# Optimization experiments

Measured on AMD Instinct MI355X. Metric: run time of the kernel, lower is better.

## Reference

```python
import jax, jax.numpy as jnp
import numpy as np

B, C, H, W = 16, 64, 32, 32
N_TOTAL = C * H * W          # 65536 flattened spatial units
N = 8192                     # samples_per_batch
EPS = 1e-12


def setup_inputs() -> dict:
    key = jax.random.key(0)
    k1, k2, k3 = jax.random.split(key, 3)
    layer_feature = jax.random.normal(k1, (B, C, H, W), dtype=jnp.float32)
    coordinates = jax.random.normal(k2, (N_TOTAL, 2), dtype=jnp.float32)
    # stand-in for torch.randperm(CHW)[:N]: unique in-range indices
    sampled_indices = jax.random.permutation(k3, N_TOTAL)[:N].astype(jnp.int64)
    return {"layer_feature": layer_feature, "coordinates": coordinates,
            "sampled_indices": sampled_indices}


def _masked_pearson(a, b, mask):
    # Pearson correlation between the masked (strict lower-triangle) entries
    cnt = jnp.sum(mask.astype(a.dtype))
    am = jnp.sum(jnp.where(mask, a, 0.0)) / cnt
    bm = jnp.sum(jnp.where(mask, b, 0.0)) / cnt
    ac = jnp.where(mask, a - am, 0.0)
    bc = jnp.where(mask, b - bm, 0.0)
    return jnp.sum(ac * bc) / (jnp.sqrt(jnp.sum(ac * ac)) * jnp.sqrt(jnp.sum(bc * bc)))


def reference(layer_feature, coordinates, sampled_indices):
    b = layer_feature.shape[0]
    feature = layer_feature.reshape(b, -1)[:, sampled_indices]   # [B, N]
    coords = coordinates[sampled_indices]                         # [N, 2]
    n = feature.shape[1]

    # distance similarity: 1 / (pdist + 1), full NxN (lower tri used)
    sq_norm = jnp.sum(coords * coords, axis=1)                    # [N]
    sq = sq_norm[:, None] + sq_norm[None, :] - 2.0 * (coords @ coords.T)
    sq = jnp.maximum(sq, 0.0)
    dist = jnp.sqrt(jnp.where(sq > EPS, sq, EPS))                 # safe sqrt
    distance_similarity = 1.0 / (dist + 1.0)                      # [N, N]

    # response similarity: corrcoef of feature.T -> NxN correlation over B
    X = feature.T                                                 # [N, B]
    Xc = X - jnp.mean(X, axis=1, keepdims=True)
    Xn = Xc / jnp.sqrt(jnp.sum(Xc * Xc, axis=1, keepdims=True))
    response_similarity = Xn @ Xn.T                               # [N, N]

    mask = jnp.tril(jnp.ones((n, n), dtype=bool), k=-1)           # strict lower tri
    similarity_alignment = _masked_pearson(response_similarity,
                                           distance_similarity, mask)
    return (1.0 - similarity_alignment) / 2.0
```

## Files before the change

kernel.cpp:

```cpp
#include <hip/hip_runtime.h>
#include <hip/hip_bf16.h>
#include <math.h>

#define NSAMP 8192
#define BATCH 16
#define CHW   65536
#define EPS_F 1e-12f

#define BT    128
#define NBT   (NSAMP / BT)
#define NINT  (NBT * (NBT - 1) / 2)
#define NBLK  (NINT + NBT)

typedef __attribute__((ext_vector_type(8))) short short8v;
typedef __attribute__((ext_vector_type(4))) float f32x4;
typedef __attribute__((ext_vector_type(2))) float f32x2;

#define OFF_XA 86016
#define OFF_C2 (OFF_XA + NSAMP * 32 * 2)

__global__ void __launch_bounds__(256)
prep_kernel(const float* __restrict__ feat, const float* __restrict__ coords,
            const int* __restrict__ sidx,
            __hip_bfloat16* __restrict__ XA, float* __restrict__ C2) {
    int t = blockIdx.x * 256 + threadIdx.x;
    int n = t >> 4, b = t & 15;
    int id = sidx[n];
    float v = feat[b * CHW + id];

    float m = v;
    m += __shfl_xor(m, 1, 16); m += __shfl_xor(m, 2, 16);
    m += __shfl_xor(m, 4, 16); m += __shfl_xor(m, 8, 16);
    float c = v - m * (1.0f / 16.0f);
    float q = c * c;
    q += __shfl_xor(q, 1, 16); q += __shfl_xor(q, 2, 16);
    q += __shfl_xor(q, 4, 16); q += __shfl_xor(q, 8, 16);
    float x = c * (1.0f / sqrtf(q));

    __hip_bfloat16 hi = __float2bfloat16(x);
    float hif = __bfloat162float(hi);
    __hip_bfloat16 lo = __float2bfloat16(x - hif);

    XA[n * 32 + b]      = hi;
    XA[n * 32 + 16 + b] = lo;
    if (b == 0) {
        float2 cc = reinterpret_cast<const float2*>(coords)[id];
        reinterpret_cast<float2*>(C2)[n] = cc;
    }
}

template<bool DIAG>
__device__ __forceinline__ void
compute_tiles(const short* __restrict__ XAs, const float* __restrict__ C2,
              int iW, int jW, int wi, int wj, int col, int kg, int rb,
              f32x2& vSa, f32x2& vSb, f32x2& vSab, f32x2& vSaa, f32x2& vSbb) {
    short8v afr[4], bhl[4], blh[4];
    f32x2 cix[4][2], ciy[4][2];
    float2 cj[4];
#pragma unroll
    for (int ti = 0; ti < 4; ++ti) {
        int rowA = iW + ti * 16 + col;
        afr[ti] = *reinterpret_cast<const short8v*>(XAs + rowA * 32 + kg * 8);
        const float4* cp =
            reinterpret_cast<const float4*>(C2 + (iW + ti * 16 + rb) * 2);
        float4 ca = cp[0], cb = cp[1];
        cix[ti][0] = (f32x2){ca.x, ca.z};  ciy[ti][0] = (f32x2){ca.y, ca.w};
        cix[ti][1] = (f32x2){cb.x, cb.z};  ciy[ti][1] = (f32x2){cb.y, cb.w};
    }
#pragma unroll
    for (int tj = 0; tj < 4; ++tj) {
        int rowB = jW + tj * 16 + col;
        bhl[tj] = *reinterpret_cast<const short8v*>(XAs + rowB * 32 + kg * 8);
        blh[tj] = *reinterpret_cast<const short8v*>(XAs + rowB * 32 + ((kg ^ 2) * 8));
        cj[tj]  = reinterpret_cast<const float2*>(C2)[rowB];
    }

#pragma unroll
    for (int tj = 0; tj < 4; ++tj) {
        const int gj = jW + tj * 16 + col;
        const f32x2 cjx = {cj[tj].x, cj[tj].x};
        const f32x2 cjy = {cj[tj].y, cj[tj].y};
        f32x4 acc[4];
#pragma unroll
        for (int ti = 0; ti < 4; ++ti) {
            if (DIAG && wi == wj && ti < tj) continue;
            f32x4 z = {0.f, 0.f, 0.f, 0.f};
            z = __builtin_amdgcn_mfma_f32_16x16x32_bf16(afr[ti], bhl[tj], z, 0, 0, 0);
            z = __builtin_amdgcn_mfma_f32_16x16x32_bf16(afr[ti], blh[tj], z, 0, 0, 0);
            acc[ti] = z;
        }
#pragma unroll
        for (int ti = 0; ti < 4; ++ti) {
            if (DIAG && wi == wj && ti < tj) continue;
            const int giB = iW + ti * 16 + rb;
#pragma unroll
            for (int p = 0; p < 2; ++p) {
                f32x2 av = {acc[ti][2 * p], acc[ti][2 * p + 1]};
                f32x2 dx = cix[ti][p] - cjx;
                f32x2 dy = ciy[ti][p] - cjy;
                f32x2 s2 = dx * dx + dy * dy;
                s2.x = fmaxf(s2.x, EPS_F);
                s2.y = fmaxf(s2.y, EPS_F);
                f32x2 d1;
                d1.x = __builtin_amdgcn_sqrtf(s2.x);
                d1.y = __builtin_amdgcn_sqrtf(s2.y);
                d1 = d1 + (f32x2){1.0f, 1.0f};
                f32x2 bb;
                bb.x = __builtin_amdgcn_rcpf(d1.x);
                bb.y = __builtin_amdgcn_rcpf(d1.y);
                f32x2 am = av;
                if (DIAG) {
                    f32x2 mk = {(giB + 2 * p + 0) > gj ? 1.0f : 0.0f,
                                (giB + 2 * p + 1) > gj ? 1.0f : 0.0f};
                    bb *= mk;
                    am *= mk;
                }
                vSa += am;
                vSb += bb;
                vSab += av * bb;
                vSaa += am * am;
                vSbb += bb * bb;
            }
        }
    }
}

template<bool DIAG>
__global__ void __launch_bounds__(256)
pair_kernel(const __hip_bfloat16* __restrict__ XA,
            const float* __restrict__ C2,
            double* __restrict__ partials) {
    int bi, bj, slot;
    if (DIAG) {
        bi = bj = blockIdx.x; slot = NINT + blockIdx.x;
    } else {
        int t = blockIdx.x;
        int e = (int)((1.0f + sqrtf(1.0f + 8.0f * (float)t)) * 0.5f);
        while (e * (e - 1) / 2 > t) --e;
        while ((e + 1) * e / 2 <= t) ++e;
        bi = e; bj = t - e * (e - 1) / 2; slot = t;
    }
    const int tid = threadIdx.x;
    const int wid = tid >> 6, l = tid & 63;
    const int wi = wid >> 1, wj = wid & 1;
    const int col = l & 15, kg = l >> 4, rb = kg * 4;

    const int iW = bi * BT + wi * 64;
    const int jW = bj * BT + wj * 64;

    f32x2 vSa = {0.f, 0.f}, vSb = {0.f, 0.f}, vSab = {0.f, 0.f};
    f32x2 vSaa = {0.f, 0.f}, vSbb = {0.f, 0.f};

    if (!(DIAG && wj > wi)) {
        const short* XAs = reinterpret_cast<const short*>(XA);
        compute_tiles<DIAG>(XAs, C2, iW, jW, wi, wj, col, kg, rb,
                            vSa, vSb, vSab, vSaa, vSbb);
    }

    double dSa  = (double)vSa.x  + (double)vSa.y;
    double dSb  = (double)vSb.x  + (double)vSb.y;
    double dSab = (double)vSab.x + (double)vSab.y;
    double dSaa = (double)vSaa.x + (double)vSaa.y;
    double dSbb = (double)vSbb.x + (double)vSbb.y;
#pragma unroll
    for (int o = 32; o > 0; o >>= 1) {
        dSa  += __shfl_down(dSa,  o, 64);
        dSb  += __shfl_down(dSb,  o, 64);
        dSab += __shfl_down(dSab, o, 64);
        dSaa += __shfl_down(dSaa, o, 64);
        dSbb += __shfl_down(dSbb, o, 64);
    }
    __shared__ double red[4][5];
    if (l == 0) {
        red[wid][0] = dSa;  red[wid][1] = dSb;  red[wid][2] = dSab;
        red[wid][3] = dSaa; red[wid][4] = dSbb;
    }
    __syncthreads();
    if (tid == 0) {
#pragma unroll
        for (int q = 0; q < 5; ++q)
            partials[slot * 5 + q] =
                red[0][q] + red[1][q] + red[2][q] + red[3][q];
    }
}

__global__ void __launch_bounds__(256)
finish_kernel(const double* __restrict__ partials, float* __restrict__ out) {
    double s0 = 0, s1 = 0, s2 = 0, s3 = 0, s4 = 0;
    for (int b = threadIdx.x; b < NBLK; b += 256) {
        s0 += partials[b * 5 + 0]; s1 += partials[b * 5 + 1];
        s2 += partials[b * 5 + 2]; s3 += partials[b * 5 + 3];
        s4 += partials[b * 5 + 4];
    }
    const int lane = threadIdx.x & 63, wid = threadIdx.x >> 6;
#pragma unroll
    for (int o = 32; o > 0; o >>= 1) {
        s0 += __shfl_down(s0, o, 64); s1 += __shfl_down(s1, o, 64);
        s2 += __shfl_down(s2, o, 64); s3 += __shfl_down(s3, o, 64);
        s4 += __shfl_down(s4, o, 64);
    }
    __shared__ double red[4][5];
    if (lane == 0) {
        red[wid][0] = s0; red[wid][1] = s1; red[wid][2] = s2;
        red[wid][3] = s3; red[wid][4] = s4;
    }
    __syncthreads();
    if (threadIdx.x == 0) {
        double Sa  = red[0][0] + red[1][0] + red[2][0] + red[3][0];
        double Sb  = red[0][1] + red[1][1] + red[2][1] + red[3][1];
        double Sab = red[0][2] + red[1][2] + red[2][2] + red[3][2];
        double Saa = red[0][3] + red[1][3] + red[2][3] + red[3][3];
        double Sbb = red[0][4] + red[1][4] + red[2][4] + red[3][4];
        const double cnt = (double)NSAMP * (double)(NSAMP - 1) * 0.5;
        double am = Sa / cnt, bm = Sb / cnt;
        double cov = Sab - cnt * am * bm;
        double va  = Saa - cnt * am * am;
        double vb  = Sbb - cnt * bm * bm;
        double corr = cov / (sqrt(va) * sqrt(vb));
        out[0] = (float)((1.0 - corr) * 0.5);
    }
}

extern "C" void kernel_launch(void* const* d_in, const int* in_sizes, int n_in,
                              void* d_out, int out_size, void* d_ws, size_t ws_size,
                              hipStream_t stream) {
    const float* feat   = (const float*)d_in[0];
    const float* coords = (const float*)d_in[1];
    const int*   sidx   = (const int*)d_in[2];
    float* out = (float*)d_out;

    double* partials = (double*)d_ws;
    __hip_bfloat16* XA = (__hip_bfloat16*)((char*)d_ws + OFF_XA);
    float* C2 = (float*)((char*)d_ws + OFF_C2);

    prep_kernel<<<NSAMP * BATCH / 256, 256, 0, stream>>>(feat, coords, sidx,
                                                         XA, C2);
    pair_kernel<false><<<NINT, 256, 0, stream>>>(XA, C2, partials);
    pair_kernel<true><<<NBT, 256, 0, stream>>>(XA, C2, partials);
    finish_kernel<<<1, 256, 0, stream>>>(partials, out);
}
```

Before: 87.48 us.

## Stage block tiles in padded LDS and fuse MFMA with epilogue

Each block now copies its 128-row A and B slices of the split-bf16 features, plus their coordinates, into padded shared memory (row stride 40 shorts) before computing. The per-wave fragment loads then read from LDS instead of global/L2, so the four waves share one copy of each tile. The MFMA and the similarity epilogue are fused per tile so no accumulator array is kept, the EPS clamp before sqrt is dropped, and launch bounds request 4 blocks per CU. The price is an extra LDS round trip and a __syncthreads per block. Without the clamp, coincident coordinates give sqrt(0) rather than sqrt(EPS), which should change the result only negligibly.

```diff
diff --git a/kernel.cpp b/kernel.cpp
--- a/kernel.cpp
+++ b/kernel.cpp
@@ -5,12 +5,13 @@
 #define NSAMP 8192
 #define BATCH 16
 #define CHW   65536
-#define EPS_F 1e-12f
 
 #define BT    128
 #define NBT   (NSAMP / BT)
 #define NINT  (NBT * (NBT - 1) / 2)
 #define NBLK  (NINT + NBT)
+
+#define LROW 40
 
 typedef __attribute__((ext_vector_type(8))) short short8v;
 typedef __attribute__((ext_vector_type(4))) float f32x4;
@@ -51,7 +52,8 @@
 
 template<bool DIAG>
 __device__ __forceinline__ void
-compute_tiles(const short* __restrict__ XAs, const float* __restrict__ C2,
+compute_tiles(const short* sA, const short* sB,
+              const float2* scA, const float2* scB,
               int iW, int jW, int wi, int wj, int col, int kg, int rb,
               f32x2& vSa, f32x2& vSb, f32x2& vSab, f32x2& vSaa, f32x2& vSbb) {
     short8v afr[4], bhl[4], blh[4];
@@ -59,20 +61,19 @@
     float2 cj[4];
 #pragma unroll
     for (int ti = 0; ti < 4; ++ti) {
-        int rowA = iW + ti * 16 + col;
-        afr[ti] = *reinterpret_cast<const short8v*>(XAs + rowA * 32 + kg * 8);
-        const float4* cp =
-            reinterpret_cast<const float4*>(C2 + (iW + ti * 16 + rb) * 2);
+        int rA = wi * 64 + ti * 16;
+        afr[ti] = *reinterpret_cast<const short8v*>(sA + (rA + col) * LROW + kg * 8);
+        const float4* cp = reinterpret_cast<const float4*>(&scA[rA + rb]);
         float4 ca = cp[0], cb = cp[1];
         cix[ti][0] = (f32x2){ca.x, ca.z};  ciy[ti][0] = (f32x2){ca.y, ca.w};
         cix[ti][1] = (f32x2){cb.x, cb.z};  ciy[ti][1] = (f32x2){cb.y, cb.w};
     }
 #pragma unroll
     for (int tj = 0; tj < 4; ++tj) {
-        int rowB = jW + tj * 16 + col;
-        bhl[tj] = *reinterpret_cast<const short8v*>(XAs + rowB * 32 + kg * 8);
-        blh[tj] = *reinterpret_cast<const short8v*>(XAs + rowB * 32 + ((kg ^ 2) * 8));
-        cj[tj]  = reinterpret_cast<const float2*>(C2)[rowB];
+        int rB = wj * 64 + tj * 16 + col;
+        bhl[tj] = *reinterpret_cast<const short8v*>(sB + rB * LROW + kg * 8);
+        blh[tj] = *reinterpret_cast<const short8v*>(sB + rB * LROW + ((kg ^ 2) * 8));
+        cj[tj]  = scB[rB];
     }
 
 #pragma unroll
@@ -80,27 +81,19 @@
         const int gj = jW + tj * 16 + col;
         const f32x2 cjx = {cj[tj].x, cj[tj].x};
         const f32x2 cjy = {cj[tj].y, cj[tj].y};
-        f32x4 acc[4];
 #pragma unroll
         for (int ti = 0; ti < 4; ++ti) {
             if (DIAG && wi == wj && ti < tj) continue;
             f32x4 z = {0.f, 0.f, 0.f, 0.f};
             z = __builtin_amdgcn_mfma_f32_16x16x32_bf16(afr[ti], bhl[tj], z, 0, 0, 0);
             z = __builtin_amdgcn_mfma_f32_16x16x32_bf16(afr[ti], blh[tj], z, 0, 0, 0);
-            acc[ti] = z;
-        }
-#pragma unroll
-        for (int ti = 0; ti < 4; ++ti) {
-            if (DIAG && wi == wj && ti < tj) continue;
             const int giB = iW + ti * 16 + rb;
 #pragma unroll
             for (int p = 0; p < 2; ++p) {
-                f32x2 av = {acc[ti][2 * p], acc[ti][2 * p + 1]};
+                f32x2 av = {z[2 * p], z[2 * p + 1]};
                 f32x2 dx = cix[ti][p] - cjx;
                 f32x2 dy = ciy[ti][p] - cjy;
                 f32x2 s2 = dx * dx + dy * dy;
-                s2.x = fmaxf(s2.x, EPS_F);
-                s2.y = fmaxf(s2.y, EPS_F);
                 f32x2 d1;
                 d1.x = __builtin_amdgcn_sqrtf(s2.x);
                 d1.y = __builtin_amdgcn_sqrtf(s2.y);
@@ -126,7 +119,7 @@
 }
 
 template<bool DIAG>
-__global__ void __launch_bounds__(256)
+__global__ void __launch_bounds__(256, 4)
 pair_kernel(const __hip_bfloat16* __restrict__ XA,
             const float* __restrict__ C2,
             double* __restrict__ partials) {
@@ -145,15 +138,39 @@
     const int wi = wid >> 1, wj = wid & 1;
     const int col = l & 15, kg = l >> 4, rb = kg * 4;
 
-    const int iW = bi * BT + wi * 64;
-    const int jW = bj * BT + wj * 64;
+    const int iBase = bi * BT, jBase = bj * BT;
+    const int iW = iBase + wi * 64;
+    const int jW = jBase + wj * 64;
+
+    __shared__ __align__(16) short  sA[BT * LROW];
+    __shared__ __align__(16) short  sB[BT * LROW];
+    __shared__ __align__(16) float2 scA[BT];
+    __shared__ __align__(16) float2 scB[BT];
+
+    const short* XAs = reinterpret_cast<const short*>(XA);
+    {
+        const int r = tid >> 1, h = tid & 1;
+        const float4* gA =
+            reinterpret_cast<const float4*>(XAs + (iBase + r) * 32 + h * 16);
+        float4 a0 = gA[0], a1 = gA[1];
+        const float4* gB =
+            reinterpret_cast<const float4*>(XAs + (jBase + r) * 32 + h * 16);
+        float4 b0 = gB[0], b1 = gB[1];
+        float4* dA = reinterpret_cast<float4*>(sA + r * LROW + h * 16);
+        dA[0] = a0; dA[1] = a1;
+        float4* dB = reinterpret_cast<float4*>(sB + r * LROW + h * 16);
+        dB[0] = b0; dB[1] = b1;
+        if (tid < BT) scA[tid] = reinterpret_cast<const float2*>(C2)[iBase + tid];
+        else          scB[tid - BT] =
+                          reinterpret_cast<const float2*>(C2)[jBase + (tid - BT)];
+    }
+    __syncthreads();
 
     f32x2 vSa = {0.f, 0.f}, vSb = {0.f, 0.f}, vSab = {0.f, 0.f};
     f32x2 vSaa = {0.f, 0.f}, vSbb = {0.f, 0.f};
 
     if (!(DIAG && wj > wi)) {
-        const short* XAs = reinterpret_cast<const short*>(XA);
-        compute_tiles<DIAG>(XAs, C2, iW, jW, wi, wj, col, kg, rb,
+        compute_tiles<DIAG>(sA, sB, scA, scB, iW, jW, wi, wj, col, kg, rb,
                             vSa, vSb, vSab, vSaa, vSbb);
     }
 
```

Result: no change. 86.41 us (-1.2%).
